# Optimization experiments

Hardware: AMD Instinct MI355X
Metric: run time of the kernel (lower is better)

Reference implementation:

```python
import jax, jax.numpy as jnp
import numpy as np

WS = 7          # window size
HN = 6          # heads
C = 192         # emb dim
SHIFT = WS >> 1
L = WS * WS


def _rel_index(ws):
    c = np.stack(np.meshgrid(np.arange(ws), np.arange(ws), indexing='ij'), -1).reshape(-1, 2)
    d = c[:, None, :] - c[None, :, :] + (ws - 1)
    return jnp.asarray(d[..., 0] * (2 * ws - 1) + d[..., 1])  # (L, L) int


def _shift_mask(ws, shift):
    # after intra-window roll by -shift, positions >= ws-shift are wrapped pixels
    r = (np.arange(ws) >= ws - shift).astype(np.int32)
    rid = (2 * r[:, None] + r[None, :]).reshape(-1)  # (L,) region id
    m = np.where(rid[:, None] != rid[None, :], -100.0, 0.0).astype(np.float32)
    return jnp.asarray(m)  # (L, L)


def _ln(x, g, b, eps=1e-5):
    m = jnp.mean(x, -1, keepdims=True)
    v = jnp.mean(jnp.square(x - m), -1, keepdims=True)
    return (x - m) * jax.lax.rsqrt(v + eps) * g + b


def _wmsa(x, qkv_w, qkv_b, proj_w, proj_b, bias_table, rel_idx, mask):
    N, wn, Lx, Cx = x.shape
    dh = Cx // HN
    qkv = x @ qkv_w + qkv_b                      # (N, wn, L, 3C)
    q, k, v = jnp.split(qkv, 3, axis=-1)
    q = q.reshape(N, wn, Lx, HN, dh) * (dh ** -0.5)
    k = k.reshape(N, wn, Lx, HN, dh)
    v = v.reshape(N, wn, Lx, HN, dh)
    a = jnp.einsum('nwqhd,nwkhd->nwhqk', q, k)   # (N, wn, H, L, L)
    a = a + jnp.transpose(bias_table[rel_idx], (2, 0, 1))  # (H, L, L) bias
    if mask is not None:
        a = a + mask                             # (L, L) broadcast
    a = jax.nn.softmax(a, axis=-1)
    o = jnp.einsum('nwhqk,nwkhd->nwqhd', a, v).reshape(N, wn, Lx, Cx)
    return o @ proj_w + proj_b


def _layer(X, g1, b1, g2, b2, qkv_w, qkv_b, proj_w, proj_b, bias_table, rel_idx,
           w1, bb1, w2, bb2, mask):
    tmp = _ln(X, g1, b1)
    tmp = _wmsa(tmp, qkv_w, qkv_b, proj_w, proj_b, bias_table, rel_idx, mask)
    X = _ln(X + tmp, g2, b2)  # drop_path is identity in eval
    h = jax.nn.gelu(X @ w1 + bb1, approximate=False)
    return X + (h @ w2 + bb2)


def setup_inputs() -> dict:
    key = jax.random.key(0)
    ks = jax.random.split(key, 16)
    N, wn = 8, 1024
    s = 0.02
    d = {}
    d['X'] = jax.random.normal(ks[0], (N, wn, L, C), jnp.float32)
    d['ln1_g'] = jnp.ones((C,), jnp.float32)
    d['ln1_b'] = jnp.zeros((C,), jnp.float32)
    d['ln2_g'] = jnp.ones((C,), jnp.float32)
    d['ln2_b'] = jnp.zeros((C,), jnp.float32)
    d['win_qkv_w'] = jax.random.normal(ks[1], (C, 3 * C), jnp.float32) * s
    d['win_qkv_b'] = jnp.zeros((3 * C,), jnp.float32)
    d['win_proj_w'] = jax.random.normal(ks[2], (C, C), jnp.float32) * s
    d['win_proj_b'] = jnp.zeros((C,), jnp.float32)
    d['win_bias'] = jax.random.normal(ks[3], ((2 * WS - 1) ** 2, HN), jnp.float32) * s
    d['swin_qkv_w'] = jax.random.normal(ks[4], (C, 3 * C), jnp.float32) * s
    d['swin_qkv_b'] = jnp.zeros((3 * C,), jnp.float32)
    d['swin_proj_w'] = jax.random.normal(ks[5], (C, C), jnp.float32) * s
    d['swin_proj_b'] = jnp.zeros((C,), jnp.float32)
    d['swin_bias'] = jax.random.normal(ks[6], ((2 * WS - 1) ** 2, HN), jnp.float32) * s
    d['mlp_w1'] = jax.random.normal(ks[7], (C, 4 * C), jnp.float32) * s
    d['mlp_b1'] = jnp.zeros((4 * C,), jnp.float32)
    d['mlp_w2'] = jax.random.normal(ks[8], (4 * C, C), jnp.float32) * s
    d['mlp_b2'] = jnp.zeros((C,), jnp.float32)
    return d


def reference(X, ln1_g, ln1_b, ln2_g, ln2_b,
              win_qkv_w, win_qkv_b, win_proj_w, win_proj_b, win_bias,
              swin_qkv_w, swin_qkv_b, swin_proj_w, swin_proj_b, swin_bias,
              mlp_w1, mlp_b1, mlp_w2, mlp_b2):
    rel_idx = _rel_index(WS)
    mask = _shift_mask(WS, SHIFT)
    N, wn = X.shape[0], X.shape[1]
    # block 1: plain window MSA
    X = _layer(X, ln1_g, ln1_b, ln2_g, ln2_b, win_qkv_w, win_qkv_b, win_proj_w,
               win_proj_b, win_bias, rel_idx, mlp_w1, mlp_b1, mlp_w2, mlp_b2, None)
    # intra-window cyclic shift (torch dims (-2,-3) = W,H axes)
    X = X.reshape(N, wn, WS, WS, C)
    X = jnp.roll(X, (-SHIFT, -SHIFT), axis=(3, 2))
    X = X.reshape(N, wn, L, C)
    # block 2: shifted window MSA with mask
    X = _layer(X, ln1_g, ln1_b, ln2_g, ln2_b, swin_qkv_w, swin_qkv_b, swin_proj_w,
               swin_proj_b, swin_bias, rel_idx, mlp_w1, mlp_b1, mlp_w2, mlp_b2, mask)
    # reverse roll — repo uses dims (-1,-2) = (C, W) axes; replicated faithfully
    X = X.reshape(N, wn, WS, WS, C)
    X = jnp.roll(X, (SHIFT, SHIFT), axis=(4, 3))
    return X.reshape(N, wn, L, C)
```

## Files before the change

kernel.cpp:

```cpp
#include <hip/hip_runtime.h>
#include <hip/hip_bf16.h>
#include <math.h>

#define NTOK 401408
#define NWIN 8192
#define NCHUNK 4
#define TOK_PER_CHUNK (NTOK / NCHUNK)
#define WIN_PER_CHUNK (NWIN / NCHUNK)

typedef __attribute__((ext_vector_type(8))) short bf16x8_t;
typedef __attribute__((ext_vector_type(4))) float f32x4_t;

__device__ __forceinline__ float bf2f(unsigned int u) {
    return __uint_as_float(u << 16);
}
__device__ __forceinline__ unsigned short f2bf(float f) {
    unsigned int x = __float_as_uint(f);
    x += 0x7fffu + ((x >> 16) & 1u);
    return (unsigned short)(x >> 16);
}
__device__ __forceinline__ unsigned int pack2bf(float a, float b) {
    return (unsigned int)f2bf(a) | ((unsigned int)f2bf(b) << 16);
}

__global__ void wt_all_kernel(const float* __restrict__ s0, const float* __restrict__ s1,
                              const float* __restrict__ s2, const float* __restrict__ s3,
                              const float* __restrict__ s4, const float* __restrict__ s5,
                              unsigned short* __restrict__ d0, unsigned short* __restrict__ d1,
                              unsigned short* __restrict__ d2, unsigned short* __restrict__ d3,
                              unsigned short* __restrict__ d4, unsigned short* __restrict__ d5) {
    int seg = blockIdx.y;
    const float* W; unsigned short* WT; int K, N;
    switch (seg) {
        case 0:  W = s0; WT = d0; K = 192; N = 576; break;
        case 1:  W = s1; WT = d1; K = 192; N = 576; break;
        case 2:  W = s2; WT = d2; K = 192; N = 192; break;
        case 3:  W = s3; WT = d3; K = 192; N = 192; break;
        case 4:  W = s4; WT = d4; K = 192; N = 768; break;
        default: W = s5; WT = d5; K = 768; N = 192; break;
    }
    int i = blockIdx.x * 256 + threadIdx.x;
    if (i >= N * K) return;
    int n = i / K, k = i - n * K;
    WT[i] = f2bf(W[(size_t)k * N + n]);
}

__global__ void bias_kernel(const float* __restrict__ bt0, const float* __restrict__ bt1,
                            float* __restrict__ bm) {
    int idx = blockIdx.x * 256 + threadIdx.x;
    int variant = blockIdx.y;
    const float* bt = variant ? bt1 : bt0;
    int r = idx & 3, lane = (idx >> 2) & 63, ni = (idx >> 8) & 3, mi = (idx >> 10) & 3, h = idx >> 12;
    int g = lane >> 4;
    int q = ni * 16 + (lane & 15);
    int k = mi * 16 + g * 4 + r;
    float v = 0.f;
    if (q < 49 && k < 49) {
        int qh = q / 7, qw = q - qh * 7, kh = k / 7, kw = k - kh * 7;
        v = bt[((qh - kh + 6) * 13 + (qw - kw + 6)) * 6 + h];
        if (variant) {
            int rq = 2 * (qh >= 4) + (qw >= 4), rk = 2 * (kh >= 4) + (kw >= 4);
            if (rq != rk) v -= 100.f;
        }
    }
    bm[(size_t)variant * 24576 + idx] = v;
}

template<int IN_BF16, int ROLL>
__global__ __launch_bounds__(256) void ln_kernel(const void* __restrict__ in,
                                                 unsigned short* __restrict__ out,
                                                 const float* __restrict__ g,
                                                 const float* __restrict__ b) {
    int t   = threadIdx.x;
    int tok = blockIdx.x * 8 + (t >> 5);
    int li  = t & 31;
    int e0  = li * 6;
    int src = tok;
    if (ROLL) {
        int win = tok / 49, p2 = tok - win * 49;
        int h = p2 / 7, w = p2 - h * 7;
        int h2 = h + 3; if (h2 >= 7) h2 -= 7;
        int w2 = w + 3; if (w2 >= 7) w2 -= 7;
        src = win * 49 + h2 * 7 + w2;
    }
    float x[6];
    if (IN_BF16) {
        const unsigned short* p = (const unsigned short*)in + (size_t)src * 192 + e0;
        unsigned int u0 = *(const unsigned int*)(p);
        unsigned int u1 = *(const unsigned int*)(p + 2);
        unsigned int u2 = *(const unsigned int*)(p + 4);
        x[0] = bf2f(u0 & 0xffffu); x[1] = bf2f(u0 >> 16);
        x[2] = bf2f(u1 & 0xffffu); x[3] = bf2f(u1 >> 16);
        x[4] = bf2f(u2 & 0xffffu); x[5] = bf2f(u2 >> 16);
    } else {
        const float* p = (const float*)in + (size_t)src * 192 + e0;
        float2 a = *(const float2*)(p);
        float2 c = *(const float2*)(p + 2);
        float2 d = *(const float2*)(p + 4);
        x[0] = a.x; x[1] = a.y; x[2] = c.x; x[3] = c.y; x[4] = d.x; x[5] = d.y;
    }
    float s = 0.f, sq = 0.f;
    #pragma unroll
    for (int j = 0; j < 6; ++j) { s += x[j]; sq += x[j] * x[j]; }
    #pragma unroll
    for (int o = 16; o; o >>= 1) { s += __shfl_xor(s, o); sq += __shfl_xor(sq, o); }
    float m   = s * (1.f / 192.f);
    float var = sq * (1.f / 192.f) - m * m;
    float r   = rsqrtf(var + 1e-5f);
    float gv[6], bv[6];
    #pragma unroll
    for (int j = 0; j < 6; ++j) { gv[j] = g[e0 + j]; bv[j] = b[e0 + j]; }
    unsigned short* q = out + (size_t)tok * 192 + e0;
    #pragma unroll
    for (int j = 0; j < 3; ++j) {
        float y0 = (x[2 * j]     - m) * r * gv[2 * j]     + bv[2 * j];
        float y1 = (x[2 * j + 1] - m) * r * gv[2 * j + 1] + bv[2 * j + 1];
        *(unsigned int*)(q + 2 * j) = pack2bf(y0, y1);
    }
}

#define EP_QKV        0
#define EP_MLP1       3
#define EP_MLP2_TRUNK 4
#define EP_MLP2_OUT   5

template<int NDIM, int KDIM, int NY, int EP>
__global__ __launch_bounds__(256) void gemm_kernel(const unsigned short* __restrict__ A,
                                                   const unsigned short* __restrict__ WT,
                                                   const float* __restrict__ bias,
                                                   const void* __restrict__ res,
                                                   void* __restrict__ out,
                                                   int row0) {
    __shared__ __align__(16) unsigned short As[128][40];
    __shared__ __align__(16) unsigned short Bs[96][40];
    int tid = threadIdx.x;
    int nwg = gridDim.x;
    int id = blockIdx.x;
    int id2 = (id & 7) * (nwg >> 3) + (id >> 3);
    int by = id2 % NY, bx = id2 / NY;
    int rowBase = bx * 128;
    int colBase = by * 96;

    int cr = tid >> 2, cp = (tid & 3) * 8;
    const unsigned short* Ab = A  + (size_t)rowBase * KDIM + cp;
    const unsigned short* Bb = WT + (size_t)colBase * KDIM + cp;

    uint4 a0, a1, b0, b1;
    const int NT = KDIM / 32;

    #define LOADK(k0)                                                          \
        do {                                                                   \
            a0 = *(const uint4*)(Ab + (size_t)cr * KDIM + (k0));               \
            a1 = *(const uint4*)(Ab + (size_t)(cr + 64) * KDIM + (k0));        \
            b0 = *(const uint4*)(Bb + (size_t)cr * KDIM + (k0));               \
            if (tid < 128) b1 = *(const uint4*)(Bb + (size_t)(cr + 64) * KDIM + (k0)); \
        } while (0)
    #define WRITEK()                                                           \
        do {                                                                   \
            *(uint4*)&As[cr][cp] = a0;                                         \
            *(uint4*)&As[cr + 64][cp] = a1;                                    \
            *(uint4*)&Bs[cr][cp] = b0;                                         \
            if (tid < 128) *(uint4*)&Bs[cr + 64][cp] = b1;                     \
        } while (0)

    LOADK(0);

    int wave = tid >> 6, lane = tid & 63;
    int wm = wave >> 1, wn = wave & 1;
    int kq = lane >> 4, lr = lane & 15;

    f32x4_t acc[4][3] = {};
    for (int kt = 0; kt < NT; ++kt) {
        __syncthreads();
        WRITEK();
        if (kt + 1 < NT) LOADK((kt + 1) * 32);
        __syncthreads();
        bf16x8_t afr[4], bfr[3];
        #pragma unroll
        for (int mi = 0; mi < 4; ++mi)
            afr[mi] = *(const bf16x8_t*)&As[wm * 64 + mi * 16 + lr][kq * 8];
        #pragma unroll
        for (int ni = 0; ni < 3; ++ni)
            bfr[ni] = *(const bf16x8_t*)&Bs[wn * 48 + ni * 16 + lr][kq * 8];
        #pragma unroll
        for (int mi = 0; mi < 4; ++mi)
            #pragma unroll
            for (int ni = 0; ni < 3; ++ni)
                acc[mi][ni] = __builtin_amdgcn_mfma_f32_16x16x32_bf16(
                    afr[mi], bfr[ni], acc[mi][ni], 0, 0, 0);
    }
    #undef LOADK
    #undef WRITEK

    const unsigned short* resb = (const unsigned short*)res;
    #pragma unroll
    for (int mi = 0; mi < 4; ++mi) {
        #pragma unroll
        for (int ni = 0; ni < 3; ++ni) {
            int col = colBase + wn * 48 + ni * 16 + lr;
            float bcol = bias[col];
            #pragma unroll
            for (int r = 0; r < 4; ++r) {
                int rloc = rowBase + wm * 64 + mi * 16 + kq * 4 + r;
                float v = acc[mi][ni][r] + bcol;
                if (EP == EP_QKV) {
                    if (colBase < 192) v *= 0.17677669529663687f;
                    ((unsigned short*)out)[(size_t)rloc * NDIM + col] = f2bf(v);
                } else if (EP == EP_MLP1) {
                    float u2 = v * (1.59576912f + 0.0713548162f * v * v);
                    float e  = __expf(u2);
                    float gl = v - v * __builtin_amdgcn_rcpf(e + 1.f);
                    ((unsigned short*)out)[(size_t)rloc * NDIM + col] = f2bf(gl);
                } else if (EP == EP_MLP2_TRUNK) {
                    v += bf2f((unsigned int)resb[(size_t)rloc * 192 + col]);
                    int grow = row0 + rloc;
                    ((unsigned short*)out)[(size_t)grow * 192 + col] = f2bf(v);
                } else {
                    v += bf2f((unsigned int)resb[(size_t)rloc * 192 + col]);
                    int grow = row0 + rloc;
                    int win = grow / 49, p2 = grow - win * 49;
                    int h = p2 / 7, w = p2 - h * 7;
                    int w2 = w + 3; if (w2 >= 7) w2 -= 7;
                    int c2 = col + 3; if (c2 >= 192) c2 -= 192;
                    ((float*)out)[((size_t)win * 49 + h * 7 + w2) * 192 + c2] = v;
                }
            }
        }
    }
}

template<int ROLLRES>
__global__ __launch_bounds__(256) void projln_kernel(const unsigned short* __restrict__ A,
                                                     const unsigned short* __restrict__ WT,
                                                     const float* __restrict__ bias,
                                                     const void* __restrict__ res,
                                                     const float* __restrict__ g2,
                                                     const float* __restrict__ b2,
                                                     unsigned short* __restrict__ out) {
    __shared__ __align__(16) unsigned short As[128][40];
    __shared__ __align__(16) unsigned short Bs[192][40];
    int tid = threadIdx.x;
    int nwg = gridDim.x;
    int id = blockIdx.x;
    int bx = (id & 7) * (nwg >> 3) + (id >> 3);
    int rowBase = bx * 128;

    int cr = tid >> 2, cp = (tid & 3) * 8;
    const unsigned short* Ab = A  + (size_t)rowBase * 192 + cp;
    const unsigned short* Bb = WT + cp;

    uint4 a0, a1, b0, b1, b2r;
    #define LOADK(k0)                                                          \
        do {                                                                   \
            a0  = *(const uint4*)(Ab + (size_t)cr * 192 + (k0));               \
            a1  = *(const uint4*)(Ab + (size_t)(cr + 64) * 192 + (k0));        \
            b0  = *(const uint4*)(Bb + (size_t)cr * 192 + (k0));               \
            b1  = *(const uint4*)(Bb + (size_t)(cr + 64) * 192 + (k0));        \
            b2r = *(const uint4*)(Bb + (size_t)(cr + 128) * 192 + (k0));       \
        } while (0)
    #define WRITEK()                                                           \
        do {                                                                   \
            *(uint4*)&As[cr][cp] = a0;                                         \
            *(uint4*)&As[cr + 64][cp] = a1;                                    \
            *(uint4*)&Bs[cr][cp] = b0;                                         \
            *(uint4*)&Bs[cr + 64][cp] = b1;                                    \
            *(uint4*)&Bs[cr + 128][cp] = b2r;                                  \
        } while (0)

    LOADK(0);

    int wave = tid >> 6, lane = tid & 63;
    int wm = wave;
    int kq = lane >> 4, lr = lane & 15;

    f32x4_t acc[2][12] = {};
    for (int kt = 0; kt < 6; ++kt) {
        __syncthreads();
        WRITEK();
        if (kt + 1 < 6) LOADK((kt + 1) * 32);
        __syncthreads();
        bf16x8_t afr[2];
        #pragma unroll
        for (int mi = 0; mi < 2; ++mi)
            afr[mi] = *(const bf16x8_t*)&As[wm * 32 + mi * 16 + lr][kq * 8];
        #pragma unroll
        for (int half = 0; half < 2; ++half) {
            bf16x8_t bfr[6];
            #pragma unroll
            for (int ni = 0; ni < 6; ++ni)
                bfr[ni] = *(const bf16x8_t*)&Bs[(half * 6 + ni) * 16 + lr][kq * 8];
            #pragma unroll
            for (int mi = 0; mi < 2; ++mi)
                #pragma unroll
                for (int ni = 0; ni < 6; ++ni)
                    acc[mi][half * 6 + ni] = __builtin_amdgcn_mfma_f32_16x16x32_bf16(
                        afr[mi], bfr[ni], acc[mi][half * 6 + ni], 0, 0, 0);
        }
    }
    #undef LOADK
    #undef WRITEK

    const float* resf = (const float*)res;
    const unsigned short* resb = (const unsigned short*)res;
    float biasv[12], g2v[12], b2v[12];
    #pragma unroll
    for (int ni = 0; ni < 12; ++ni) {
        int col = ni * 16 + lr;
        biasv[ni] = bias[col]; g2v[ni] = g2[col]; b2v[ni] = b2[col];
    }

    #pragma unroll
    for (int mi = 0; mi < 2; ++mi) {
        #pragma unroll
        for (int r = 0; r < 4; ++r) {
            int rloc = rowBase + wm * 32 + mi * 16 + kq * 4 + r;
            size_t rsrc = rloc;
            if (ROLLRES) {
                int win = rloc / 49, p2 = rloc - win * 49;
                int h = p2 / 7, w = p2 - h * 7;
                int h2 = h + 3; if (h2 >= 7) h2 -= 7;
                int w2 = w + 3; if (w2 >= 7) w2 -= 7;
                rsrc = (size_t)win * 49 + h2 * 7 + w2;
            }
            float v[12], s = 0.f, sq = 0.f;
            #pragma unroll
            for (int ni = 0; ni < 12; ++ni) {
                int col = ni * 16 + lr;
                float t = acc[mi][ni][r] + biasv[ni];
                t += ROLLRES ? bf2f((unsigned int)resb[rsrc * 192 + col])
                             : resf[rsrc * 192 + col];
                v[ni] = t; s += t; sq += t * t;
            }
            s  += __shfl_xor(s, 1);  s  += __shfl_xor(s, 2);
            s  += __shfl_xor(s, 4);  s  += __shfl_xor(s, 8);
            sq += __shfl_xor(sq, 1); sq += __shfl_xor(sq, 2);
            sq += __shfl_xor(sq, 4); sq += __shfl_xor(sq, 8);
            float mean = s * (1.f / 192.f);
            float var  = sq * (1.f / 192.f) - mean * mean;
            float rstd = rsqrtf(var + 1e-5f);
            unsigned short* op = out + (size_t)rloc * 192;
            #pragma unroll
            for (int ni = 0; ni < 12; ++ni) {
                int col = ni * 16 + lr;
                op[col] = f2bf((v[ni] - mean) * rstd * g2v[ni] + b2v[ni]);
            }
        }
    }
}

__global__ __launch_bounds__(64) void attn_kernel(const unsigned short* __restrict__ qkv,
                                                  const float* __restrict__ bm,
                                                  unsigned short* __restrict__ outp,
                                                  int win0) {
    __shared__ unsigned short P[64][72];
    __shared__ unsigned short VT[32][72];
    int head = blockIdx.x, wloc = blockIdx.y;
    int lane = threadIdx.x;
    int g = lane >> 4, lr = lane & 15;
    const unsigned short* base = qkv + (size_t)wloc * 49 * 576;

    for (int i = lane; i < 256; i += 64) {
        int tok = i >> 2, seg = i & 3;
        uint4 u = make_uint4(0u, 0u, 0u, 0u);
        if (tok < 49)
            u = *(const uint4*)(base + (size_t)tok * 576 + 384 + head * 32 + seg * 8);
        const unsigned short* us = (const unsigned short*)&u;
        #pragma unroll
        for (int j = 0; j < 8; ++j) VT[seg * 8 + j][tok] = us[j];
    }

    bf16x8_t kf[4], qf[4];
    #pragma unroll
    for (int mi = 0; mi < 4; ++mi) {
        int tok = mi * 16 + lr; if (tok > 48) tok = 48;
        kf[mi] = *(const bf16x8_t*)(base + (size_t)tok * 576 + 192 + head * 32 + g * 8);
    }
    #pragma unroll
    for (int ni = 0; ni < 4; ++ni) {
        int tok = ni * 16 + lr; if (tok > 48) tok = 48;
        qf[ni] = *(const bf16x8_t*)(base + (size_t)tok * 576 + head * 32 + g * 8);
    }

    const float* bmh = bm + (size_t)head * 4096;
    f32x4_t acc[4][4];
    #pragma unroll
    for (int mi = 0; mi < 4; ++mi)
        #pragma unroll
        for (int ni = 0; ni < 4; ++ni)
            acc[mi][ni] = *(const f32x4_t*)(bmh + ((mi * 4 + ni) * 64 + lane) * 4);
    __builtin_amdgcn_s_setprio(1);
    #pragma unroll
    for (int mi = 0; mi < 4; ++mi)
        #pragma unroll
        for (int ni = 0; ni < 4; ++ni)
            acc[mi][ni] = __builtin_amdgcn_mfma_f32_16x16x32_bf16(kf[mi], qf[ni], acc[mi][ni], 0, 0, 0);
    __builtin_amdgcn_s_setprio(0);

    float inv[4];
    #pragma unroll
    for (int ni = 0; ni < 4; ++ni) {
        float mx = -1e30f;
        #pragma unroll
        for (int mi = 0; mi < 3; ++mi)
            #pragma unroll
            for (int r = 0; r < 4; ++r) mx = fmaxf(mx, acc[mi][ni][r]);
        mx = fmaxf(mx, (g == 0) ? acc[3][ni][0] : -1e30f);
        mx = fmaxf(mx, __shfl_xor(mx, 16));
        mx = fmaxf(mx, __shfl_xor(mx, 32));
        float p[16], ss = 0.f;
        #pragma unroll
        for (int mi = 0; mi < 3; ++mi)
            #pragma unroll
            for (int r = 0; r < 4; ++r) {
                float e = __expf(acc[mi][ni][r] - mx);
                p[mi * 4 + r] = e; ss += e;
            }
        float e48 = (g == 0) ? __expf(acc[3][ni][0] - mx) : 0.f;
        p[12] = e48; p[13] = p[14] = p[15] = 0.f; ss += e48;
        ss += __shfl_xor(ss, 16);
        ss += __shfl_xor(ss, 32);
        inv[ni] = 1.f / ss;
        int q = ni * 16 + lr;
        #pragma unroll
        for (int mi = 0; mi < 4; ++mi) {
            *(unsigned int*)&P[q][mi * 16 + g * 4]     = pack2bf(p[mi * 4 + 0], p[mi * 4 + 1]);
            *(unsigned int*)&P[q][mi * 16 + g * 4 + 2] = pack2bf(p[mi * 4 + 2], p[mi * 4 + 3]);
        }
    }
    __syncthreads();

    f32x4_t oacc[2][4] = {};
    #pragma unroll
    for (int kt = 0; kt < 2; ++kt) {
        bf16x8_t va[2], pb[4];
        #pragma unroll
        for (int mt = 0; mt < 2; ++mt)
            va[mt] = *(const bf16x8_t*)&VT[mt * 16 + lr][kt * 32 + g * 8];
        #pragma unroll
        for (int nt = 0; nt < 4; ++nt)
            pb[nt] = *(const bf16x8_t*)&P[nt * 16 + lr][kt * 32 + g * 8];
        __builtin_amdgcn_s_setprio(1);
        #pragma unroll
        for (int mt = 0; mt < 2; ++mt)
            #pragma unroll
            for (int nt = 0; nt < 4; ++nt)
                oacc[mt][nt] = __builtin_amdgcn_mfma_f32_16x16x32_bf16(va[mt], pb[nt], oacc[mt][nt], 0, 0, 0);
        __builtin_amdgcn_s_setprio(0);
    }

    #pragma unroll
    for (int nt = 0; nt < 4; ++nt) {
        int q = nt * 16 + lr;
        if (q < 49) {
            size_t tokg = (size_t)(win0 + wloc) * 49 + q;
            unsigned short* op = outp + tokg * 192 + head * 32;
            #pragma unroll
            for (int mt = 0; mt < 2; ++mt) {
                int d0 = mt * 16 + g * 4;
                float a0 = oacc[mt][nt][0] * inv[nt], a1 = oacc[mt][nt][1] * inv[nt];
                float a2 = oacc[mt][nt][2] * inv[nt], a3 = oacc[mt][nt][3] * inv[nt];
                *(unsigned int*)(op + d0)     = pack2bf(a0, a1);
                *(unsigned int*)(op + d0 + 2) = pack2bf(a2, a3);
            }
        }
    }
}

extern "C" void kernel_launch(void* const* d_in, const int* in_sizes, int n_in,
                              void* d_out, int out_size, void* d_ws, size_t ws_size,
                              hipStream_t stream) {
    (void)in_sizes; (void)n_in; (void)out_size; (void)ws_size;
    const float* X     = (const float*)d_in[0];
    const float* ln1_g = (const float*)d_in[1];
    const float* ln1_b = (const float*)d_in[2];
    const float* ln2_g = (const float*)d_in[3];
    const float* ln2_b = (const float*)d_in[4];
    const float* qkv_w[2]  = { (const float*)d_in[5],  (const float*)d_in[10] };
    const float* qkv_b[2]  = { (const float*)d_in[6],  (const float*)d_in[11] };
    const float* proj_w[2] = { (const float*)d_in[7],  (const float*)d_in[12] };
    const float* proj_b[2] = { (const float*)d_in[8],  (const float*)d_in[13] };
    const float* btab[2]   = { (const float*)d_in[9],  (const float*)d_in[14] };
    const float* w1 = (const float*)d_in[15];
    const float* b1 = (const float*)d_in[16];
    const float* w2 = (const float*)d_in[17];
    const float* b2 = (const float*)d_in[18];

    char* p = (char*)d_ws;
    auto takeb = [&](size_t bytes) -> char* {
        char* r = p;
        p += (bytes + 255) & ~(size_t)255;
        return r;
    };
    auto take = [&](size_t elems) -> unsigned short* {
        return (unsigned short*)takeb(elems * 2);
    };
    unsigned short* WTq[2]; unsigned short* WTp[2];
    WTq[0] = take(576 * 192); WTp[0] = take(192 * 192);
    WTq[1] = take(576 * 192); WTp[1] = take(192 * 192);
    unsigned short* WT1 = take(768 * 192);
    unsigned short* WT2 = take(192 * 768);
    float* biasM = (float*)takeb(2 * 24576 * sizeof(float));
    unsigned short* B0 = take((size_t)NTOK * 192);
    unsigned short* B1 = take((size_t)TOK_PER_CHUNK * 768);
    unsigned short* TK = take((size_t)NTOK * 192);

    wt_all_kernel<<<dim3(576, 6), dim3(256), 0, stream>>>(
        qkv_w[0], qkv_w[1], proj_w[0], proj_w[1], w1, w2,
        WTq[0], WTq[1], WTp[0], WTp[1], WT1, WT2);
    bias_kernel<<<dim3(96, 2), dim3(256), 0, stream>>>(btab[0], btab[1], biasM);

    for (int blk = 0; blk < 2; ++blk) {
        if (blk == 0)
            ln_kernel<0, 0><<<dim3(NTOK / 8), dim3(256), 0, stream>>>((const void*)X, B0, ln1_g, ln1_b);
        else
            ln_kernel<1, 1><<<dim3(NTOK / 8), dim3(256), 0, stream>>>((const void*)TK, B0, ln1_g, ln1_b);

        for (int c = 0; c < NCHUNK; ++c) {
            int row0 = c * TOK_PER_CHUNK;
            gemm_kernel<576, 192, 6, EP_QKV><<<dim3((TOK_PER_CHUNK / 128) * 6), dim3(256), 0, stream>>>(
                B0 + (size_t)row0 * 192, WTq[blk], qkv_b[blk], nullptr, (void*)B1, row0);
            attn_kernel<<<dim3(6, WIN_PER_CHUNK), dim3(64), 0, stream>>>(
                B1, biasM + (size_t)blk * 24576, B0, c * WIN_PER_CHUNK);
        }

        if (blk == 0)
            projln_kernel<0><<<dim3(NTOK / 128), dim3(256), 0, stream>>>(
                B0, WTp[blk], proj_b[blk], (const void*)X, ln2_g, ln2_b, B0);
        else
            projln_kernel<1><<<dim3(NTOK / 128), dim3(256), 0, stream>>>(
                B0, WTp[blk], proj_b[blk], (const void*)TK, ln2_g, ln2_b, B0);

        for (int c = 0; c < NCHUNK; ++c) {
            int row0 = c * TOK_PER_CHUNK;
            gemm_kernel<768, 192, 8, EP_MLP1><<<dim3((TOK_PER_CHUNK / 128) * 8), dim3(256), 0, stream>>>(
                B0 + (size_t)row0 * 192, WT1, b1, nullptr, (void*)B1, row0);
            if (blk == 0)
                gemm_kernel<192, 768, 2, EP_MLP2_TRUNK><<<dim3((TOK_PER_CHUNK / 128) * 2), dim3(256), 0, stream>>>(
                    B1, WT2, b2, (const void*)(B0 + (size_t)row0 * 192), (void*)TK, row0);
            else
                gemm_kernel<192, 768, 2, EP_MLP2_OUT><<<dim3((TOK_PER_CHUNK / 128) * 2), dim3(256), 0, stream>>>(
                    B1, WT2, b2, (const void*)(B0 + (size_t)row0 * 192), (void*)d_out, row0);
        }
    }
}
```

Measured before the change: 2.471 ms.

## Stage GEMM tiles via direct global-to-LDS loads with double buffering and XOR swizzle

The generic GEMM kernel now loads A and B tiles straight from global memory into LDS with global_load_lds instead of staging them through registers. It double-buffers LDS so the next K-slice loads while the current one is multiplied, which removes one barrier per iteration. The padded row layout is replaced by an XOR swizzle to avoid LDS bank conflicts. The synchronisation looks thin: only one __syncthreads per iteration and no explicit wait on the async LDS loads, so the correctness of the ordering rests on the barrier draining them.

```diff
diff --git a/kernel.cpp b/kernel.cpp
--- a/kernel.cpp
+++ b/kernel.cpp
@@ -22,6 +22,11 @@
 __device__ __forceinline__ unsigned int pack2bf(float a, float b) {
     return (unsigned int)f2bf(a) | ((unsigned int)f2bf(b) << 16);
 }
+
+#define GLOAD16(gsrc, ldst)                                                        \
+    __builtin_amdgcn_global_load_lds(                                              \
+        (const __attribute__((address_space(1))) unsigned int*)(gsrc),             \
+        (__attribute__((address_space(3))) unsigned int*)(ldst), 16, 0, 0)
 
 __global__ void wt_all_kernel(const float* __restrict__ s0, const float* __restrict__ s1,
                               const float* __restrict__ s2, const float* __restrict__ s3,
@@ -131,8 +136,8 @@
                                                    const void* __restrict__ res,
                                                    void* __restrict__ out,
                                                    int row0) {
-    __shared__ __align__(16) unsigned short As[128][40];
-    __shared__ __align__(16) unsigned short Bs[96][40];
+    __shared__ __align__(16) unsigned short As[2][128][32];
+    __shared__ __align__(16) unsigned short Bs[2][96][32];
     int tid = threadIdx.x;
     int nwg = gridDim.x;
     int id = blockIdx.x;
@@ -141,56 +146,52 @@
     int rowBase = bx * 128;
     int colBase = by * 96;
 
-    int cr = tid >> 2, cp = (tid & 3) * 8;
-    const unsigned short* Ab = A  + (size_t)rowBase * KDIM + cp;
-    const unsigned short* Bb = WT + (size_t)colBase * KDIM + cp;
-
-    uint4 a0, a1, b0, b1;
+    int wave = tid >> 6, lane = tid & 63;
+    int grow  = lane >> 2;
+    int gslot = (lane & 3) ^ ((lane >> 3) & 3);
+    const unsigned short* Ag = A  + (size_t)rowBase * KDIM + gslot * 8;
+    const unsigned short* Bg = WT + (size_t)colBase * KDIM + gslot * 8;
+
     const int NT = KDIM / 32;
 
-    #define LOADK(k0)                                                          \
-        do {                                                                   \
-            a0 = *(const uint4*)(Ab + (size_t)cr * KDIM + (k0));               \
-            a1 = *(const uint4*)(Ab + (size_t)(cr + 64) * KDIM + (k0));        \
-            b0 = *(const uint4*)(Bb + (size_t)cr * KDIM + (k0));               \
-            if (tid < 128) b1 = *(const uint4*)(Bb + (size_t)(cr + 64) * KDIM + (k0)); \
+    #define STAGE(buf, k0)                                                            \
+        do {                                                                          \
+            int qa = wave * 32;                                                       \
+            GLOAD16(Ag + (size_t)(qa + grow) * KDIM + (k0),      &As[buf][qa][0]);    \
+            GLOAD16(Ag + (size_t)(qa + 16 + grow) * KDIM + (k0), &As[buf][qa + 16][0]); \
+            if (wave < 3) {                                                           \
+                GLOAD16(Bg + (size_t)(qa + grow) * KDIM + (k0),      &Bs[buf][qa][0]);    \
+                GLOAD16(Bg + (size_t)(qa + 16 + grow) * KDIM + (k0), &Bs[buf][qa + 16][0]); \
+            }                                                                         \
         } while (0)
-    #define WRITEK()                                                           \
-        do {                                                                   \
-            *(uint4*)&As[cr][cp] = a0;                                         \
-            *(uint4*)&As[cr + 64][cp] = a1;                                    \
-            *(uint4*)&Bs[cr][cp] = b0;                                         \
-            if (tid < 128) *(uint4*)&Bs[cr + 64][cp] = b1;                     \
-        } while (0)
-
-    LOADK(0);
-
-    int wave = tid >> 6, lane = tid & 63;
+
+    STAGE(0, 0);
+
     int wm = wave >> 1, wn = wave & 1;
     int kq = lane >> 4, lr = lane & 15;
+    int sa = (kq ^ ((lr >> 1) & 3)) * 8;
 
     f32x4_t acc[4][3] = {};
+    int buf = 0;
     for (int kt = 0; kt < NT; ++kt) {
         __syncthreads();
-        WRITEK();
-        if (kt + 1 < NT) LOADK((kt + 1) * 32);
-        __syncthreads();
+        if (kt + 1 < NT) STAGE(buf ^ 1, (kt + 1) * 32);
         bf16x8_t afr[4], bfr[3];
         #pragma unroll
         for (int mi = 0; mi < 4; ++mi)
-            afr[mi] = *(const bf16x8_t*)&As[wm * 64 + mi * 16 + lr][kq * 8];
+            afr[mi] = *(const bf16x8_t*)&As[buf][wm * 64 + mi * 16 + lr][sa];
         #pragma unroll
         for (int ni = 0; ni < 3; ++ni)
-            bfr[ni] = *(const bf16x8_t*)&Bs[wn * 48 + ni * 16 + lr][kq * 8];
+            bfr[ni] = *(const bf16x8_t*)&Bs[buf][wn * 48 + ni * 16 + lr][sa];
         #pragma unroll
         for (int mi = 0; mi < 4; ++mi)
             #pragma unroll
             for (int ni = 0; ni < 3; ++ni)
                 acc[mi][ni] = __builtin_amdgcn_mfma_f32_16x16x32_bf16(
                     afr[mi], bfr[ni], acc[mi][ni], 0, 0, 0);
-    }
-    #undef LOADK
-    #undef WRITEK
+        buf ^= 1;
+    }
+    #undef STAGE
 
     const unsigned short* resb = (const unsigned short*)res;
     #pragma unroll
@@ -213,12 +214,12 @@
                     ((unsigned short*)out)[(size_t)rloc * NDIM + col] = f2bf(gl);
                 } else if (EP == EP_MLP2_TRUNK) {
                     v += bf2f((unsigned int)resb[(size_t)rloc * 192 + col]);
-                    int grow = row0 + rloc;
-                    ((unsigned short*)out)[(size_t)grow * 192 + col] = f2bf(v);
+                    int grow2 = row0 + rloc;
+                    ((unsigned short*)out)[(size_t)grow2 * 192 + col] = f2bf(v);
                 } else {
                     v += bf2f((unsigned int)resb[(size_t)rloc * 192 + col]);
-                    int grow = row0 + rloc;
-                    int win = grow / 49, p2 = grow - win * 49;
+                    int grow2 = row0 + rloc;
+                    int win = grow2 / 49, p2 = grow2 - win * 49;
                     int h = p2 / 7, w = p2 - h * 7;
                     int w2 = w + 3; if (w2 >= 7) w2 -= 7;
                     int c2 = col + 3; if (c2 >= 192) c2 -= 192;
```

After: 2.607 ms. +5.5%, slower.
